# Optimization experiments

Measured on AMD Instinct MI355X. Metric: run time of the kernel, lower is better.

The kernel has to match this reference:

```python
import jax, jax.numpy as jnp
import numpy as np
from jax import lax

H = 2048      # d_inner
N = 8         # half of d_state (conjugate-pair complex modes)
B, L, D_MODEL = 4, 4096, 1024
D_CONV = 4


def setup_inputs() -> dict:
    key = jax.random.key(0)
    ks = jax.random.split(key, 10)
    hidden_states = jax.random.normal(ks[0], (B, L, D_MODEL), dtype=jnp.float32)
    W_in = jax.random.normal(ks[1], (2 * H, D_MODEL), dtype=jnp.float32) / np.sqrt(D_MODEL)
    conv_w = jax.random.normal(ks[2], (H, D_CONV), dtype=jnp.float32) / np.sqrt(D_CONV)
    conv_b = jax.random.normal(ks[3], (H,), dtype=jnp.float32) * 0.1
    # S4D params: dt ~ loguniform(1e-3, 1e-1); A = -0.5 + i*pi*n (legs-ish diag init)
    u = jax.random.uniform(ks[4], (H,), dtype=jnp.float32)
    log_dt = jnp.log(1e-3) + u * (jnp.log(1e-1) - jnp.log(1e-3))
    log_A_real = jnp.log(0.5 * jnp.ones((H, N), dtype=jnp.float32))
    A_imag = jnp.pi * jnp.broadcast_to(jnp.arange(N, dtype=jnp.float32), (H, N)).copy()
    C_re = jax.random.normal(ks[5], (H, N), dtype=jnp.float32)
    C_im = jax.random.normal(ks[6], (H, N), dtype=jnp.float32)
    D = jnp.ones((H,), dtype=jnp.float32)
    W_out = jax.random.normal(ks[7], (D_MODEL, H), dtype=jnp.float32) / np.sqrt(H)
    return dict(hidden_states=hidden_states, W_in=W_in, conv_w=conv_w, conv_b=conv_b,
                log_dt=log_dt, log_A_real=log_A_real, A_imag=A_imag,
                C_re=C_re, C_im=C_im, D=D, W_out=W_out)


def _s4d_kernel(log_dt, log_A_real, A_imag, C_re, C_im, L):
    # S4D (diagonal SSM) convolution kernel, ZOH-style discretization.
    dt = jnp.exp(log_dt)                       # (H,)
    A = -jnp.exp(log_A_real) + 1j * A_imag      # (H,N) complex
    C = C_re + 1j * C_im                        # (H,N)
    dtA = dt[:, None] * A                       # (H,N)
    Ct = C * (jnp.exp(dtA) - 1.0) / A           # (H,N)
    t = jnp.arange(L, dtype=jnp.float32)
    vand = jnp.exp(dtA[:, :, None] * t)         # (H,N,L) Vandermonde
    return 2.0 * jnp.einsum('hn,hnl->hl', Ct, vand).real  # (H,L)


def reference(hidden_states, W_in, conv_w, conv_b, log_dt, log_A_real, A_imag, C_re, C_im, D, W_out):
    B, L, _ = hidden_states.shape
    # in_proj (no bias): (B,L,D) -> (B, 2H, L)
    xz = jnp.einsum('bld,ed->bel', hidden_states, W_in)
    x, z = jnp.split(xz, 2, axis=1)             # each (B,H,L)
    # causal depthwise conv1d + SiLU
    w = conv_w.shape[-1]
    xp = jnp.pad(x, ((0, 0), (0, 0), (w - 1, 0)))
    x = lax.conv_general_dilated(xp, conv_w[:, None, :], (1,), 'VALID',
                                 dimension_numbers=('NCH', 'OIH', 'NCH'),
                                 feature_group_count=x.shape[1])
    x = jax.nn.silu(x + conv_b[None, :, None])
    # S4 FFT long convolution + D skip
    k = _s4d_kernel(log_dt, log_A_real, A_imag, C_re, C_im, L)  # (H,L)
    n = 2 * L
    y = jnp.fft.irfft(jnp.fft.rfft(x, n=n) * jnp.fft.rfft(k, n=n), n=n)[..., :L]
    y = y + x * D[None, :, None]
    # SiLU gate and out_proj
    y = y * jax.nn.silu(z)
    return jnp.einsum('bhl,dh->bld', y, W_out)
```

## Files before the change

### kernel.cpp

```cpp
#include <hip/hip_runtime.h>
#include <hip/hip_bf16.h>
#include <math.h>

#define H_DIM 2048
#define N_ST 8
#define B_SZ 4
#define L_SEQ 4096
#define DMODEL 1024
#define DCONV 4
#define CL 128
#define NC (L_SEQ / CL)

typedef __bf16 bf16x8 __attribute__((ext_vector_type(8)));
typedef __bf16 bf16x4 __attribute__((ext_vector_type(4)));
typedef float f32x4 __attribute__((ext_vector_type(4)));

typedef const unsigned int __attribute__((address_space(1)))* gptr_t;
typedef unsigned int __attribute__((address_space(3)))* lptr_t;

__device__ __forceinline__ void gl_lds16(const __bf16* g, __bf16* l) {
    __builtin_amdgcn_global_load_lds((gptr_t)g, (lptr_t)l, 16, 0, 0);
}

#define WS_XZ     0
#define WS_COEF   16777216
#define WS_STATES 16875520
#define WS_HF     17924096
#define WS_WIF    24215552
#define WS_WOH    30507008
#define WS_WOL    31555584
#define WS_YTL    32604160

__global__ __launch_bounds__(256) void cvt_split4(const float* __restrict__ s,
                                                  __bf16* __restrict__ h,
                                                  __bf16* __restrict__ l, int n4) {
    int i = blockIdx.x * 256 + threadIdx.x;
    if (i >= n4) return;
    float4 v = ((const float4*)s)[i];
    float vv[4] = {v.x, v.y, v.z, v.w};
    bf16x4 hv, lv;
#pragma unroll
    for (int j = 0; j < 4; ++j) {
        __bf16 hb = (__bf16)vv[j];
        hv[j] = hb;
        lv[j] = (__bf16)(vv[j] - (float)hb);
    }
    *(bf16x4*)&h[(size_t)i * 4] = hv;
    *(bf16x4*)&l[(size_t)i * 4] = lv;
}

template <int BSIDE>
__global__ __launch_bounds__(256) void cvt_fuse(const float* __restrict__ s,
                                                __bf16* __restrict__ d, int nOct) {
    int i = blockIdx.x * 256 + threadIdx.x;
    if (i >= nOct) return;
    int row = i >> 7, ko = i & 127;
    const float* p = s + (size_t)row * 1024 + ko * 8;
    float4 v0 = *(const float4*)p;
    float4 v1 = *(const float4*)(p + 4);
    float vv[8] = {v0.x, v0.y, v0.z, v0.w, v1.x, v1.y, v1.z, v1.w};
    bf16x8 hv, lv;
#pragma unroll
    for (int j = 0; j < 8; ++j) {
        __bf16 hb = (__bf16)vv[j];
        hv[j] = hb;
        lv[j] = (__bf16)(vv[j] - (float)hb);
    }
    __bf16* o = d + (size_t)row * 3072 + ko * 24;
    if (BSIDE) {
        *(bf16x8*)(o) = hv; *(bf16x8*)(o + 8) = lv; *(bf16x8*)(o + 16) = hv;
    } else {
        *(bf16x8*)(o) = hv; *(bf16x8*)(o + 8) = hv; *(bf16x8*)(o + 16) = lv;
    }
}

__global__ void coef_kernel(const float* __restrict__ log_dt,
                            const float* __restrict__ log_A_real,
                            const float* __restrict__ A_imag,
                            const float* __restrict__ C_re,
                            const float* __restrict__ C_im,
                            float* __restrict__ coef) {
    int i = blockIdx.x * blockDim.x + threadIdx.x;
    if (i >= H_DIM * N_ST) return;
    int h = i >> 3;
    float dt = expf(log_dt[h]);
    float Ar = -expf(log_A_real[i]);
    float Ai = A_imag[i];
    float er = expf(dt * Ar);
    float ang = dt * Ai;
    float wr = er * cosf(ang);
    float wi = er * sinf(ang);
    float den = Ar * Ar + Ai * Ai;
    float qr = ((wr - 1.f) * Ar + wi * Ai) / den;
    float qi = (wi * Ar - (wr - 1.f) * Ai) / den;
    float Cr = C_re[i], Ci = C_im[i];
    float Ctr = Cr * qr - Ci * qi;
    float Cti = Cr * qi + Ci * qr;
    float eCL = expf((float)CL * dt * Ar);
    float aCL = (float)CL * dt * Ai;
    float pr = eCL * cosf(aCL);
    float pi = eCL * sinf(aCL);
    const int HN = H_DIM * N_ST;
    coef[i]          = wr;
    coef[HN + i]     = wi;
    coef[2 * HN + i] = Ctr;
    coef[3 * HN + i] = Cti;
    coef[4 * HN + i] = pr;
    coef[5 * HN + i] = pi;
}

__global__ __launch_bounds__(512, 2) void gemm_f256p(const __bf16* __restrict__ A,
                                                     const __bf16* __restrict__ B,
                                                     float* __restrict__ C,
                                                     int K, int ldc) {
    __shared__ __bf16 sA[32768], sB[32768];
    const int tid = threadIdx.x;
    const int lane = tid & 63;
    const int wid = tid >> 6;
    const int wrw = wid >> 2, wcw = wid & 3;
    const int bm = blockIdx.y, bn = blockIdx.x;

    f32x4 acc[8][4];
#pragma unroll
    for (int m = 0; m < 8; ++m)
#pragma unroll
        for (int n = 0; n < 4; ++n) acc[m][n] = (f32x4){0.f, 0.f, 0.f, 0.f};

    const int kb = lane >> 4, rr = lane & 15;

    const int f0 = tid, f1 = 512 + tid;
    const int kA0 = f0 >> 8, rA0 = f0 & 255;
    const int kA1 = f1 >> 8, rA1 = f1 & 255;
    const size_t gA0 = (size_t)(bm * 256 + rA0) * K;
    const size_t gA1 = (size_t)(bm * 256 + rA1) * K;
    const size_t gB0 = (size_t)(bn * 256 + rA0) * K;
    const size_t gB1 = (size_t)(bn * 256 + rA1) * K;
    const int dst0 = kA0 * 2048 + rA0 * 8;
    const int dst1 = kA1 * 2048 + rA1 * 8;

    auto stageA = [&](int t, int ks) {
        const int base = (t & 1) * 16384 + ks * 8192;
        const size_t go = (size_t)t * 64 + ks * 32;
        gl_lds16(A + gA0 + go + kA0 * 8, &sA[base + dst0]);
        gl_lds16(A + gA1 + go + kA1 * 8, &sA[base + dst1]);
    };
    auto stageB = [&](int t, int ks) {
        const int base = (t & 1) * 16384 + ks * 8192;
        const size_t go = (size_t)t * 64 + ks * 32;
        gl_lds16(B + gB0 + go + kA0 * 8, &sB[base + dst0]);
        gl_lds16(B + gB1 + go + kA1 * 8, &sB[base + dst1]);
    };

    const int nt = K >> 6;
    stageA(0, 0); stageB(0, 0); stageA(0, 1); stageB(0, 1);
    asm volatile("s_waitcnt vmcnt(0)" ::: "memory");
    __builtin_amdgcn_s_barrier();
    __builtin_amdgcn_sched_barrier(0);

#pragma unroll 1
    for (int t = 0; t < nt; ++t) {
        const int par = (t & 1) * 16384;
        const bool pf = (t + 1 < nt);
        bf16x8 fB[4], fA[4];

        {
            const int bA = par, bB = par;
#pragma unroll
            for (int n = 0; n < 4; ++n)
                fB[n] = *(const bf16x8*)&sB[bB + kb * 2048 + (wcw * 64 + n * 16 + rr) * 8];
#pragma unroll
            for (int m = 0; m < 4; ++m)
                fA[m] = *(const bf16x8*)&sA[bA + kb * 2048 + (wrw * 128 + m * 16 + rr) * 8];
            if (pf) stageA(t + 1, 0);
            __builtin_amdgcn_s_barrier();
            asm volatile("s_waitcnt lgkmcnt(0)" ::: "memory");
            __builtin_amdgcn_sched_barrier(0);
            __builtin_amdgcn_s_setprio(1);
#pragma unroll
            for (int m = 0; m < 4; ++m)
#pragma unroll
                for (int n = 0; n < 4; ++n)
                    acc[m][n] = __builtin_amdgcn_mfma_f32_16x16x32_bf16(fA[m], fB[n], acc[m][n], 0, 0, 0);
            __builtin_amdgcn_s_setprio(0);
            __builtin_amdgcn_s_barrier();
            __builtin_amdgcn_sched_barrier(0);
        }
        {
            const int bA = par;
#pragma unroll
            for (int m = 0; m < 4; ++m)
                fA[m] = *(const bf16x8*)&sA[bA + kb * 2048 + (wrw * 128 + 64 + m * 16 + rr) * 8];
            if (pf) stageB(t + 1, 0);
            __builtin_amdgcn_s_barrier();
            asm volatile("s_waitcnt lgkmcnt(0)" ::: "memory");
            __builtin_amdgcn_sched_barrier(0);
            __builtin_amdgcn_s_setprio(1);
#pragma unroll
            for (int m = 0; m < 4; ++m)
#pragma unroll
                for (int n = 0; n < 4; ++n)
                    acc[4 + m][n] = __builtin_amdgcn_mfma_f32_16x16x32_bf16(fA[m], fB[n], acc[4 + m][n], 0, 0, 0);
            __builtin_amdgcn_s_setprio(0);
            if (pf) asm volatile("s_waitcnt vmcnt(4)" ::: "memory");
            else    asm volatile("s_waitcnt vmcnt(0)" ::: "memory");
            __builtin_amdgcn_s_barrier();
            __builtin_amdgcn_sched_barrier(0);
        }
        {
            const int bA = par + 8192, bB = par + 8192;
#pragma unroll
            for (int n = 0; n < 4; ++n)
                fB[n] = *(const bf16x8*)&sB[bB + kb * 2048 + (wcw * 64 + n * 16 + rr) * 8];
#pragma unroll
            for (int m = 0; m < 4; ++m)
                fA[m] = *(const bf16x8*)&sA[bA + kb * 2048 + (wrw * 128 + m * 16 + rr) * 8];
            if (pf) stageA(t + 1, 1);
            __builtin_amdgcn_s_barrier();
            asm volatile("s_waitcnt lgkmcnt(0)" ::: "memory");
            __builtin_amdgcn_sched_barrier(0);
            __builtin_amdgcn_s_setprio(1);
#pragma unroll
            for (int m = 0; m < 4; ++m)
#pragma unroll
                for (int n = 0; n < 4; ++n)
                    acc[m][n] = __builtin_amdgcn_mfma_f32_16x16x32_bf16(fA[m], fB[n], acc[m][n], 0, 0, 0);
            __builtin_amdgcn_s_setprio(0);
            __builtin_amdgcn_s_barrier();
            __builtin_amdgcn_sched_barrier(0);
        }
        {
            const int bA = par + 8192;
#pragma unroll
            for (int m = 0; m < 4; ++m)
                fA[m] = *(const bf16x8*)&sA[bA + kb * 2048 + (wrw * 128 + 64 + m * 16 + rr) * 8];
            if (pf) stageB(t + 1, 1);
            __builtin_amdgcn_s_barrier();
            asm volatile("s_waitcnt lgkmcnt(0)" ::: "memory");
            __builtin_amdgcn_sched_barrier(0);
            __builtin_amdgcn_s_setprio(1);
#pragma unroll
            for (int m = 0; m < 4; ++m)
#pragma unroll
                for (int n = 0; n < 4; ++n)
                    acc[4 + m][n] = __builtin_amdgcn_mfma_f32_16x16x32_bf16(fA[m], fB[n], acc[4 + m][n], 0, 0, 0);
            __builtin_amdgcn_s_setprio(0);
            if (pf) asm volatile("s_waitcnt vmcnt(4)" ::: "memory");
            else    asm volatile("s_waitcnt vmcnt(0)" ::: "memory");
            __builtin_amdgcn_s_barrier();
            __builtin_amdgcn_sched_barrier(0);
        }
    }

    const int rq = lane >> 4;
#pragma unroll
    for (int m = 0; m < 8; ++m)
#pragma unroll
        for (int n = 0; n < 4; ++n) {
            int col = bn * 256 + wcw * 64 + n * 16 + rr;
            int row0 = bm * 256 + wrw * 128 + m * 16 + rq * 4;
#pragma unroll
            for (int j = 0; j < 4; ++j)
                C[(size_t)(row0 + j) * ldc + col] = acc[m][n][j];
        }
}

__global__ __launch_bounds__(512, 1) void gemm_s128w(const __bf16* __restrict__ Ah,
                                                     const __bf16* __restrict__ Al,
                                                     const __bf16* __restrict__ Bh,
                                                     const __bf16* __restrict__ Bl,
                                                     float* __restrict__ C,
                                                     int K, int ldc) {
    __shared__ __bf16 sAh[2][2][4096], sAl[2][2][4096];
    __shared__ __bf16 sBh[2][2][4096], sBl[2][2][4096];
    const int tid = threadIdx.x;
    const int lane = tid & 63;
    const int wid = tid >> 6;
    const int wrw = wid >> 2;
    const int wcw = wid & 3;
    const int bm = blockIdx.y, bn = blockIdx.x;

    f32x4 acc[4][2];
#pragma unroll
    for (int m = 0; m < 4; ++m)
#pragma unroll
        for (int n = 0; n < 2; ++n) acc[m][n] = (f32x4){0.f, 0.f, 0.f, 0.f};

    const int kb = lane >> 4, rr = lane & 15;

    const int kbs = tid >> 7, rw = tid & 127;
    const size_t gAr = (size_t)(bm * 128 + rw) * K;
    const size_t gBr = (size_t)(bn * 128 + rw) * K;
    const int dd = kbs * 1024 + rw * 8;

    auto stA = [&](int t, int ks) {
        const int par = t & 1;
        const size_t go = (size_t)t * 64 + ks * 32 + kbs * 8;
        gl_lds16(Ah + gAr + go, &sAh[par][ks][dd]);
        gl_lds16(Al + gAr + go, &sAl[par][ks][dd]);
    };
    auto stB = [&](int t, int ks) {
        const int par = t & 1;
        const size_t go = (size_t)t * 64 + ks * 32 + kbs * 8;
        gl_lds16(Bh + gBr + go, &sBh[par][ks][dd]);
        gl_lds16(Bl + gBr + go, &sBl[par][ks][dd]);
    };

    const int nt = K >> 6;
    stA(0, 0); stB(0, 0); stA(0, 1); stB(0, 1);
    asm volatile("s_waitcnt vmcnt(0)" ::: "memory");
    __builtin_amdgcn_s_barrier();
    __builtin_amdgcn_sched_barrier(0);

    bf16x8 fAh[4], fAl[4], fBh[2], fBl[2];

#pragma unroll 1
    for (int t = 0; t < nt; ++t) {
        const int par = t & 1;
        const bool pf = (t + 1 < nt);

        {
#pragma unroll
            for (int n = 0; n < 2; ++n) {
                const int off = kb * 1024 + (wcw * 32 + n * 16 + rr) * 8;
                fBh[n] = *(const bf16x8*)&sBh[par][0][off];
                fBl[n] = *(const bf16x8*)&sBl[par][0][off];
            }
#pragma unroll
            for (int m = 0; m < 4; ++m) {
                const int off = kb * 1024 + (wrw * 64 + m * 16 + rr) * 8;
                fAh[m] = *(const bf16x8*)&sAh[par][0][off];
                fAl[m] = *(const bf16x8*)&sAl[par][0][off];
            }
            if (pf) stA(t + 1, 0);
            __builtin_amdgcn_s_barrier();
            asm volatile("s_waitcnt lgkmcnt(0)" ::: "memory");
            __builtin_amdgcn_sched_barrier(0);
            __builtin_amdgcn_s_setprio(1);
#pragma unroll
            for (int m = 0; m < 2; ++m)
#pragma unroll
                for (int n = 0; n < 2; ++n) {
                    acc[m][n] = __builtin_amdgcn_mfma_f32_16x16x32_bf16(fAh[m], fBh[n], acc[m][n], 0, 0, 0);
                    acc[m][n] = __builtin_amdgcn_mfma_f32_16x16x32_bf16(fAh[m], fBl[n], acc[m][n], 0, 0, 0);
                    acc[m][n] = __builtin_amdgcn_mfma_f32_16x16x32_bf16(fAl[m], fBh[n], acc[m][n], 0, 0, 0);
                }
            __builtin_amdgcn_s_setprio(0);
            __builtin_amdgcn_s_barrier();
            __builtin_amdgcn_sched_barrier(0);
        }
        {
            if (pf) stB(t + 1, 0);
            __builtin_amdgcn_s_barrier();
            __builtin_amdgcn_sched_barrier(0);
            __builtin_amdgcn_s_setprio(1);
#pragma unroll
            for (int m = 2; m < 4; ++m)
#pragma unroll
                for (int n = 0; n < 2; ++n) {
                    acc[m][n] = __builtin_amdgcn_mfma_f32_16x16x32_bf16(fAh[m], fBh[n], acc[m][n], 0, 0, 0);
                    acc[m][n] = __builtin_amdgcn_mfma_f32_16x16x32_bf16(fAh[m], fBl[n], acc[m][n], 0, 0, 0);
                    acc[m][n] = __builtin_amdgcn_mfma_f32_16x16x32_bf16(fAl[m], fBh[n], acc[m][n], 0, 0, 0);
                }
            __builtin_amdgcn_s_setprio(0);
            if (pf) asm volatile("s_waitcnt vmcnt(4)" ::: "memory");
            else    asm volatile("s_waitcnt vmcnt(0)" ::: "memory");
            __builtin_amdgcn_s_barrier();
            __builtin_amdgcn_sched_barrier(0);
        }
        {
#pragma unroll
            for (int n = 0; n < 2; ++n) {
                const int off = kb * 1024 + (wcw * 32 + n * 16 + rr) * 8;
                fBh[n] = *(const bf16x8*)&sBh[par][1][off];
                fBl[n] = *(const bf16x8*)&sBl[par][1][off];
            }
#pragma unroll
            for (int m = 0; m < 4; ++m) {
                const int off = kb * 1024 + (wrw * 64 + m * 16 + rr) * 8;
                fAh[m] = *(const bf16x8*)&sAh[par][1][off];
                fAl[m] = *(const bf16x8*)&sAl[par][1][off];
            }
            if (pf) stA(t + 1, 1);
            __builtin_amdgcn_s_barrier();
            asm volatile("s_waitcnt lgkmcnt(0)" ::: "memory");
            __builtin_amdgcn_sched_barrier(0);
            __builtin_amdgcn_s_setprio(1);
#pragma unroll
            for (int m = 0; m < 2; ++m)
#pragma unroll
                for (int n = 0; n < 2; ++n) {
                    acc[m][n] = __builtin_amdgcn_mfma_f32_16x16x32_bf16(fAh[m], fBh[n], acc[m][n], 0, 0, 0);
                    acc[m][n] = __builtin_amdgcn_mfma_f32_16x16x32_bf16(fAh[m], fBl[n], acc[m][n], 0, 0, 0);
                    acc[m][n] = __builtin_amdgcn_mfma_f32_16x16x32_bf16(fAl[m], fBh[n], acc[m][n], 0, 0, 0);
                }
            __builtin_amdgcn_s_setprio(0);
            __builtin_amdgcn_s_barrier();
            __builtin_amdgcn_sched_barrier(0);
        }
        {
            if (pf) stB(t + 1, 1);
            __builtin_amdgcn_s_barrier();
            __builtin_amdgcn_sched_barrier(0);
            __builtin_amdgcn_s_setprio(1);
#pragma unroll
            for (int m = 2; m < 4; ++m)
#pragma unroll
                for (int n = 0; n < 2; ++n) {
                    acc[m][n] = __builtin_amdgcn_mfma_f32_16x16x32_bf16(fAh[m], fBh[n], acc[m][n], 0, 0, 0);
                    acc[m][n] = __builtin_amdgcn_mfma_f32_16x16x32_bf16(fAh[m], fBl[n], acc[m][n], 0, 0, 0);
                    acc[m][n] = __builtin_amdgcn_mfma_f32_16x16x32_bf16(fAl[m], fBh[n], acc[m][n], 0, 0, 0);
                }
            __builtin_amdgcn_s_setprio(0);
            if (pf) asm volatile("s_waitcnt vmcnt(4)" ::: "memory");
            else    asm volatile("s_waitcnt vmcnt(0)" ::: "memory");
            __builtin_amdgcn_s_barrier();
            __builtin_amdgcn_sched_barrier(0);
        }
    }

    const int rq = lane >> 4;
#pragma unroll
    for (int m = 0; m < 4; ++m)
#pragma unroll
        for (int n = 0; n < 2; ++n) {
            int col = bn * 128 + wcw * 32 + n * 16 + rr;
            int row0 = bm * 128 + wrw * 64 + m * 16 + rq * 4;
#pragma unroll
            for (int j = 0; j < 4; ++j)
                C[(size_t)(row0 + j) * ldc + col] = acc[m][n][j];
        }
}

__global__ __launch_bounds__(256) void scan_phase1(const float* __restrict__ xz,
                                                   const float* __restrict__ coef,
                                                   const float* __restrict__ conv_w,
                                                   const float* __restrict__ conv_b,
                                                   float* __restrict__ states) {
    int t = blockIdx.x * 256 + threadIdx.x;
    int c = t & (NC - 1);
    int h = t >> 5;

    const int HN = H_DIM * N_ST;
    float wr[N_ST], wi[N_ST];
#pragma unroll
    for (int n = 0; n < N_ST; ++n) {
        wr[n] = coef[h * N_ST + n];
        wi[n] = coef[HN + h * N_ST + n];
    }
    float cw0 = conv_w[h * 4 + 0], cw1 = conv_w[h * 4 + 1];
    float cw2 = conv_w[h * 4 + 2], cw3 = conv_w[h * 4 + 3];
    float cb = conv_b[h];

    const float* xrow = xz + (size_t)h * L_SEQ + c * CL;
    float x3 = 0.f, x2 = 0.f, x1 = 0.f;
    if (c > 0) {
        float4 p = *(const float4*)(xrow - 4);
        x3 = p.y; x2 = p.z; x1 = p.w;
    }

    float sr[N_ST], si[N_ST];
#pragma unroll
    for (int n = 0; n < N_ST; ++n) { sr[n] = 0.f; si[n] = 0.f; }

    for (int j = 0; j < CL; j += 4) {
        float4 v = *(const float4*)(xrow + j);
        float xv[4] = {v.x, v.y, v.z, v.w};
#pragma unroll
        for (int k = 0; k < 4; ++k) {
            float u = cw0 * x3 + cw1 * x2 + cw2 * x1 + cw3 * xv[k] + cb;
            float xc = u / (1.f + __expf(-u));
            x3 = x2; x2 = x1; x1 = xv[k];
#pragma unroll
            for (int n = 0; n < N_ST; ++n) {
                float nr = wr[n] * sr[n] - wi[n] * si[n] + xc;
                float ni = wr[n] * si[n] + wi[n] * sr[n];
                sr[n] = nr; si[n] = ni;
            }
        }
    }
    float* st = states + (size_t)t * (N_ST * 2);
#pragma unroll
    for (int n = 0; n < N_ST; ++n) { st[2 * n] = sr[n]; st[2 * n + 1] = si[n]; }
}

__global__ __launch_bounds__(256) void scan_phase2(const float* __restrict__ coef,
                                                   float* __restrict__ states) {
    int h = blockIdx.x * 256 + threadIdx.x;
    if (h >= H_DIM) return;
    const int HN = H_DIM * N_ST;
    float pr[N_ST], pi[N_ST];
#pragma unroll
    for (int n = 0; n < N_ST; ++n) {
        pr[n] = coef[4 * HN + h * N_ST + n];
        pi[n] = coef[5 * HN + h * N_ST + n];
    }
    float sr[N_ST], si[N_ST];
#pragma unroll
    for (int n = 0; n < N_ST; ++n) { sr[n] = 0.f; si[n] = 0.f; }
    float* base = states + (size_t)h * NC * (N_ST * 2);
    for (int c = 0; c < NC; ++c) {
        float* st = base + c * (N_ST * 2);
#pragma unroll
        for (int n = 0; n < N_ST; ++n) {
            float lr = st[2 * n], li = st[2 * n + 1];
            st[2 * n] = sr[n]; st[2 * n + 1] = si[n];
            float nr = pr[n] * sr[n] - pi[n] * si[n] + lr;
            float ni = pr[n] * si[n] + pi[n] * sr[n] + li;
            sr[n] = nr; si[n] = ni;
        }
    }
}

__global__ __launch_bounds__(256) void scan_phase3t(const float* __restrict__ xz,
                                                    const float* __restrict__ coef,
                                                    const float* __restrict__ conv_w,
                                                    const float* __restrict__ conv_b,
                                                    const float* __restrict__ Dvec,
                                                    const float* __restrict__ states,
                                                    __bf16* __restrict__ th,
                                                    __bf16* __restrict__ tl) {
    const int lane = threadIdx.x & 63;
    const int wv = threadIdx.x >> 6;
    const int c = blockIdx.x * 4 + wv;
    const int h = blockIdx.y * 64 + lane;
    const int t = h * NC + c;

    const int HN = H_DIM * N_ST;
    float wr[N_ST], wi[N_ST], Ctr[N_ST], Cti[N_ST];
#pragma unroll
    for (int n = 0; n < N_ST; ++n) {
        wr[n]  = coef[h * N_ST + n];
        wi[n]  = coef[HN + h * N_ST + n];
        Ctr[n] = coef[2 * HN + h * N_ST + n];
        Cti[n] = coef[3 * HN + h * N_ST + n];
    }
    float cw0 = conv_w[h * 4 + 0], cw1 = conv_w[h * 4 + 1];
    float cw2 = conv_w[h * 4 + 2], cw3 = conv_w[h * 4 + 3];
    float cb = conv_b[h];
    float Dh = Dvec[h];

    const float* xrow = xz + (size_t)h * L_SEQ + c * CL;
    const float* zrow = xz + (size_t)(H_DIM + h) * L_SEQ + c * CL;

    float x3 = 0.f, x2 = 0.f, x1 = 0.f;
    if (c > 0) {
        float4 p = *(const float4*)(xrow - 4);
        x3 = p.y; x2 = p.z; x1 = p.w;
    }

    const float* st = states + (size_t)t * (N_ST * 2);
    float sr[N_ST], si[N_ST];
#pragma unroll
    for (int n = 0; n < N_ST; ++n) { sr[n] = st[2 * n]; si[n] = st[2 * n + 1]; }

    __bf16* thp = th + (size_t)(c * CL) * H_DIM + h;
    __bf16* tlp = tl + (size_t)(c * CL) * H_DIM + h;

    for (int j = 0; j < CL; j += 4) {
        float4 v = *(const float4*)(xrow + j);
        float4 zv = *(const float4*)(zrow + j);
        float xv[4] = {v.x, v.y, v.z, v.w};
        float zz[4] = {zv.x, zv.y, zv.z, zv.w};
#pragma unroll
        for (int k = 0; k < 4; ++k) {
            float u = cw0 * x3 + cw1 * x2 + cw2 * x1 + cw3 * xv[k] + cb;
            float xc = u / (1.f + __expf(-u));
            x3 = x2; x2 = x1; x1 = xv[k];
            float accy = 0.f;
#pragma unroll
            for (int n = 0; n < N_ST; ++n) {
                float nr = wr[n] * sr[n] - wi[n] * si[n] + xc;
                float ni = wr[n] * si[n] + wi[n] * sr[n];
                sr[n] = nr; si[n] = ni;
                accy += Ctr[n] * nr - Cti[n] * ni;
            }
            float yv = 2.f * accy + Dh * xc;
            float g = zz[k] / (1.f + __expf(-zz[k]));
            float val = yv * g;
            __bf16 hb = (__bf16)val;
            __bf16 lb = (__bf16)(val - (float)hb);
            thp[(size_t)(j + k) * H_DIM] = hb;
            tlp[(size_t)(j + k) * H_DIM] = lb;
        }
    }
}

extern "C" void kernel_launch(void* const* d_in, const int* in_sizes, int n_in,
                              void* d_out, int out_size, void* d_ws, size_t ws_size,
                              hipStream_t stream) {
    const float* hid        = (const float*)d_in[0];
    const float* W_in       = (const float*)d_in[1];
    const float* conv_w     = (const float*)d_in[2];
    const float* conv_b     = (const float*)d_in[3];
    const float* log_dt     = (const float*)d_in[4];
    const float* log_A_real = (const float*)d_in[5];
    const float* A_imag     = (const float*)d_in[6];
    const float* C_re       = (const float*)d_in[7];
    const float* C_im       = (const float*)d_in[8];
    const float* Dv         = (const float*)d_in[9];
    const float* W_out      = (const float*)d_in[10];
    float* out = (float*)d_out;
    float* ws  = (float*)d_ws;

    float* xz      = ws + WS_XZ;
    float* coef    = ws + WS_COEF;
    float* states  = ws + WS_STATES;
    __bf16* Hf     = (__bf16*)(ws + WS_HF);
    __bf16* WiF    = (__bf16*)(ws + WS_WIF);
    __bf16* Woh    = (__bf16*)(ws + WS_WOH);
    __bf16* Wol    = (__bf16*)(ws + WS_WOL);
    __bf16* yTh    = (__bf16*)(ws + WS_HF);
    __bf16* yTl    = (__bf16*)(ws + WS_YTL);

    coef_kernel<<<(H_DIM * N_ST + 255) / 256, 256, 0, stream>>>(
        log_dt, log_A_real, A_imag, C_re, C_im, coef);

    const int wOct = 2 * H_DIM * DMODEL / 8;
    cvt_fuse<0><<<(wOct + 255) / 256, 256, 0, stream>>>(W_in, WiF, wOct);
    cvt_split4<<<(DMODEL * H_DIM / 4 + 255) / 256, 256, 0, stream>>>(W_out, Woh, Wol, DMODEL * H_DIM / 4);

    const int nscan = H_DIM * NC;
    const int hOct = L_SEQ * DMODEL / 8;
    dim3 gIn(L_SEQ / 256, 2 * H_DIM / 256);
    dim3 gOut(DMODEL / 128, L_SEQ / 128);
    dim3 gP3(NC / 4, H_DIM / 64);

    for (int b = 0; b < B_SZ; ++b) {
        const float* hid_b = hid + (size_t)b * L_SEQ * DMODEL;
        float* out_b = out + (size_t)b * L_SEQ * DMODEL;

        cvt_fuse<1><<<(hOct + 255) / 256, 256, 0, stream>>>(hid_b, Hf, hOct);
        gemm_f256p<<<gIn, 512, 0, stream>>>(WiF, Hf, xz, 3 * DMODEL, L_SEQ);
        scan_phase1<<<nscan / 256, 256, 0, stream>>>(xz, coef, conv_w, conv_b, states);
        scan_phase2<<<(H_DIM + 255) / 256, 256, 0, stream>>>(coef, states);
        scan_phase3t<<<gP3, 256, 0, stream>>>(xz, coef, conv_w, conv_b, Dv, states, yTh, yTl);
        gemm_s128w<<<gOut, 512, 0, stream>>>(yTh, yTl, Woh, Wol, out_b, H_DIM, DMODEL);
    }
}
```

Measured before the change: 1.399 ms.

## Replace 256x256 in_proj GEMM with 128x128 tile, 4-wave kernel

Replaces the 512-thread, 256x256-tile input projection GEMM with a 256-thread, 128x128-tile version that uses a smaller LDS footprint and a 2x2 wave layout. Fragments of A and B are now loaded once per k-substep and reused across two MFMA phases instead of being reloaded. The grid grows fourfold, giving more blocks to fill the CUs. In exchange, each block reuses each loaded tile across fewer outputs, so global/L2 traffic per FLOP goes up.

```diff
diff --git a/kernel.cpp b/kernel.cpp
--- a/kernel.cpp
+++ b/kernel.cpp
@@ -109,75 +109,75 @@
     coef[5 * HN + i] = pi;
 }
 
-__global__ __launch_bounds__(512, 2) void gemm_f256p(const __bf16* __restrict__ A,
-                                                     const __bf16* __restrict__ B,
-                                                     float* __restrict__ C,
-                                                     int K, int ldc) {
-    __shared__ __bf16 sA[32768], sB[32768];
+__global__ __launch_bounds__(256, 2) void gemm_g128(const __bf16* __restrict__ A,
+                                                    const __bf16* __restrict__ B,
+                                                    float* __restrict__ C,
+                                                    int K, int ldc) {
+    __shared__ __bf16 sA[2][2][4096], sB[2][2][4096];
     const int tid = threadIdx.x;
     const int lane = tid & 63;
     const int wid = tid >> 6;
-    const int wrw = wid >> 2, wcw = wid & 3;
+    const int wrw = wid >> 1, wcw = wid & 1;
     const int bm = blockIdx.y, bn = blockIdx.x;
 
-    f32x4 acc[8][4];
-#pragma unroll
-    for (int m = 0; m < 8; ++m)
+    f32x4 acc[4][4];
+#pragma unroll
+    for (int m = 0; m < 4; ++m)
 #pragma unroll
         for (int n = 0; n < 4; ++n) acc[m][n] = (f32x4){0.f, 0.f, 0.f, 0.f};
 
     const int kb = lane >> 4, rr = lane & 15;
 
-    const int f0 = tid, f1 = 512 + tid;
-    const int kA0 = f0 >> 8, rA0 = f0 & 255;
-    const int kA1 = f1 >> 8, rA1 = f1 & 255;
-    const size_t gA0 = (size_t)(bm * 256 + rA0) * K;
-    const size_t gA1 = (size_t)(bm * 256 + rA1) * K;
-    const size_t gB0 = (size_t)(bn * 256 + rA0) * K;
-    const size_t gB1 = (size_t)(bn * 256 + rA1) * K;
-    const int dst0 = kA0 * 2048 + rA0 * 8;
-    const int dst1 = kA1 * 2048 + rA1 * 8;
-
-    auto stageA = [&](int t, int ks) {
-        const int base = (t & 1) * 16384 + ks * 8192;
+    const int o0 = tid, o1 = 256 + tid;
+    const int ko0 = o0 >> 7, rw0 = o0 & 127;
+    const int ko1 = o1 >> 7, rw1 = o1 & 127;
+    const size_t gA0 = (size_t)(bm * 128 + rw0) * K;
+    const size_t gA1 = (size_t)(bm * 128 + rw1) * K;
+    const size_t gB0 = (size_t)(bn * 128 + rw0) * K;
+    const size_t gB1 = (size_t)(bn * 128 + rw1) * K;
+    const int d0 = ko0 * 1024 + rw0 * 8;
+    const int d1 = ko1 * 1024 + rw1 * 8;
+
+    auto stA = [&](int t, int ks) {
+        const int par = t & 1;
         const size_t go = (size_t)t * 64 + ks * 32;
-        gl_lds16(A + gA0 + go + kA0 * 8, &sA[base + dst0]);
-        gl_lds16(A + gA1 + go + kA1 * 8, &sA[base + dst1]);
+        gl_lds16(A + gA0 + go + ko0 * 8, &sA[par][ks][d0]);
+        gl_lds16(A + gA1 + go + ko1 * 8, &sA[par][ks][d1]);
     };
-    auto stageB = [&](int t, int ks) {
-        const int base = (t & 1) * 16384 + ks * 8192;
+    auto stB = [&](int t, int ks) {
+        const int par = t & 1;
         const size_t go = (size_t)t * 64 + ks * 32;
-        gl_lds16(B + gB0 + go + kA0 * 8, &sB[base + dst0]);
-        gl_lds16(B + gB1 + go + kA1 * 8, &sB[base + dst1]);
+        gl_lds16(B + gB0 + go + ko0 * 8, &sB[par][ks][d0]);
+        gl_lds16(B + gB1 + go + ko1 * 8, &sB[par][ks][d1]);
     };
 
     const int nt = K >> 6;
-    stageA(0, 0); stageB(0, 0); stageA(0, 1); stageB(0, 1);
+    stA(0, 0); stB(0, 0); stA(0, 1); stB(0, 1);
     asm volatile("s_waitcnt vmcnt(0)" ::: "memory");
     __builtin_amdgcn_s_barrier();
     __builtin_amdgcn_sched_barrier(0);
 
+    bf16x8 fA[4], fB[4];
+
 #pragma unroll 1
     for (int t = 0; t < nt; ++t) {
-        const int par = (t & 1) * 16384;
+        const int par = t & 1;
         const bool pf = (t + 1 < nt);
-        bf16x8 fB[4], fA[4];
-
-        {
-            const int bA = par, bB = par;
+
+        {
 #pragma unroll
             for (int n = 0; n < 4; ++n)
-                fB[n] = *(const bf16x8*)&sB[bB + kb * 2048 + (wcw * 64 + n * 16 + rr) * 8];
+                fB[n] = *(const bf16x8*)&sB[par][0][kb * 1024 + (wcw * 64 + n * 16 + rr) * 8];
 #pragma unroll
             for (int m = 0; m < 4; ++m)
-                fA[m] = *(const bf16x8*)&sA[bA + kb * 2048 + (wrw * 128 + m * 16 + rr) * 8];
-            if (pf) stageA(t + 1, 0);
+                fA[m] = *(const bf16x8*)&sA[par][0][kb * 1024 + (wrw * 64 + m * 16 + rr) * 8];
+            if (pf) stA(t + 1, 0);
             __builtin_amdgcn_s_barrier();
             asm volatile("s_waitcnt lgkmcnt(0)" ::: "memory");
             __builtin_amdgcn_sched_barrier(0);
             __builtin_amdgcn_s_setprio(1);
 #pragma unroll
-            for (int m = 0; m < 4; ++m)
+            for (int m = 0; m < 2; ++m)
 #pragma unroll
                 for (int n = 0; n < 4; ++n)
                     acc[m][n] = __builtin_amdgcn_mfma_f32_16x16x32_bf16(fA[m], fB[n], acc[m][n], 0, 0, 0);
@@ -186,20 +186,15 @@
             __builtin_amdgcn_sched_barrier(0);
         }
         {
-            const int bA = par;
-#pragma unroll
-            for (int m = 0; m < 4; ++m)
-                fA[m] = *(const bf16x8*)&sA[bA + kb * 2048 + (wrw * 128 + 64 + m * 16 + rr) * 8];
-            if (pf) stageB(t + 1, 0);
-            __builtin_amdgcn_s_barrier();
-            asm volatile("s_waitcnt lgkmcnt(0)" ::: "memory");
-            __builtin_amdgcn_sched_barrier(0);
-            __builtin_amdgcn_s_setprio(1);
-#pragma unroll
-            for (int m = 0; m < 4; ++m)
+            if (pf) stB(t + 1, 0);
+            __builtin_amdgcn_s_barrier();
+            __builtin_amdgcn_sched_barrier(0);
+            __builtin_amdgcn_s_setprio(1);
+#pragma unroll
+            for (int m = 2; m < 4; ++m)
 #pragma unroll
                 for (int n = 0; n < 4; ++n)
-                    acc[4 + m][n] = __builtin_amdgcn_mfma_f32_16x16x32_bf16(fA[m], fB[n], acc[4 + m][n], 0, 0, 0);
+                    acc[m][n] = __builtin_amdgcn_mfma_f32_16x16x32_bf16(fA[m], fB[n], acc[m][n], 0, 0, 0);
             __builtin_amdgcn_s_setprio(0);
             if (pf) asm volatile("s_waitcnt vmcnt(4)" ::: "memory");
             else    asm volatile("s_waitcnt vmcnt(0)" ::: "memory");
@@ -207,20 +202,19 @@
             __builtin_amdgcn_sched_barrier(0);
         }
         {
-            const int bA = par + 8192, bB = par + 8192;
 #pragma unroll
             for (int n = 0; n < 4; ++n)
-                fB[n] = *(const bf16x8*)&sB[bB + kb * 2048 + (wcw * 64 + n * 16 + rr) * 8];
+                fB[n] = *(const bf16x8*)&sB[par][1][kb * 1024 + (wcw * 64 + n * 16 + rr) * 8];
 #pragma unroll
             for (int m = 0; m < 4; ++m)
-                fA[m] = *(const bf16x8*)&sA[bA + kb * 2048 + (wrw * 128 + m * 16 + rr) * 8];
-            if (pf) stageA(t + 1, 1);
+                fA[m] = *(const bf16x8*)&sA[par][1][kb * 1024 + (wrw * 64 + m * 16 + rr) * 8];
+            if (pf) stA(t + 1, 1);
             __builtin_amdgcn_s_barrier();
             asm volatile("s_waitcnt lgkmcnt(0)" ::: "memory");
             __builtin_amdgcn_sched_barrier(0);
             __builtin_amdgcn_s_setprio(1);
 #pragma unroll
-            for (int m = 0; m < 4; ++m)
+            for (int m = 0; m < 2; ++m)
 #pragma unroll
                 for (int n = 0; n < 4; ++n)
                     acc[m][n] = __builtin_amdgcn_mfma_f32_16x16x32_bf16(fA[m], fB[n], acc[m][n], 0, 0, 0);
@@ -229,20 +223,15 @@
             __builtin_amdgcn_sched_barrier(0);
         }
         {
-            const int bA = par + 8192;
-#pragma unroll
-            for (int m = 0; m < 4; ++m)
-                fA[m] = *(const bf16x8*)&sA[bA + kb * 2048 + (wrw * 128 + 64 + m * 16 + rr) * 8];
-            if (pf) stageB(t + 1, 1);
-            __builtin_amdgcn_s_barrier();
-            asm volatile("s_waitcnt lgkmcnt(0)" ::: "memory");
-            __builtin_amdgcn_sched_barrier(0);
-            __builtin_amdgcn_s_setprio(1);
-#pragma unroll
-            for (int m = 0; m < 4; ++m)
+            if (pf) stB(t + 1, 1);
+            __builtin_amdgcn_s_barrier();
+            __builtin_amdgcn_sched_barrier(0);
+            __builtin_amdgcn_s_setprio(1);
+#pragma unroll
+            for (int m = 2; m < 4; ++m)
 #pragma unroll
                 for (int n = 0; n < 4; ++n)
-                    acc[4 + m][n] = __builtin_amdgcn_mfma_f32_16x16x32_bf16(fA[m], fB[n], acc[4 + m][n], 0, 0, 0);
+                    acc[m][n] = __builtin_amdgcn_mfma_f32_16x16x32_bf16(fA[m], fB[n], acc[m][n], 0, 0, 0);
             __builtin_amdgcn_s_setprio(0);
             if (pf) asm volatile("s_waitcnt vmcnt(4)" ::: "memory");
             else    asm volatile("s_waitcnt vmcnt(0)" ::: "memory");
@@ -253,11 +242,11 @@
 
     const int rq = lane >> 4;
 #pragma unroll
-    for (int m = 0; m < 8; ++m)
+    for (int m = 0; m < 4; ++m)
 #pragma unroll
         for (int n = 0; n < 4; ++n) {
-            int col = bn * 256 + wcw * 64 + n * 16 + rr;
-            int row0 = bm * 256 + wrw * 128 + m * 16 + rq * 4;
+            int col = bn * 128 + wcw * 64 + n * 16 + rr;
+            int row0 = bm * 128 + wrw * 64 + m * 16 + rq * 4;
 #pragma unroll
             for (int j = 0; j < 4; ++j)
                 C[(size_t)(row0 + j) * ldc + col] = acc[m][n][j];
@@ -621,7 +610,7 @@
 
     const int nscan = H_DIM * NC;
     const int hOct = L_SEQ * DMODEL / 8;
-    dim3 gIn(L_SEQ / 256, 2 * H_DIM / 256);
+    dim3 gIn(L_SEQ / 128, 2 * H_DIM / 128);
     dim3 gOut(DMODEL / 128, L_SEQ / 128);
     dim3 gP3(NC / 4, H_DIM / 64);
 
@@ -630,7 +619,7 @@
         float* out_b = out + (size_t)b * L_SEQ * DMODEL;
 
         cvt_fuse<1><<<(hOct + 255) / 256, 256, 0, stream>>>(hid_b, Hf, hOct);
-        gemm_f256p<<<gIn, 512, 0, stream>>>(WiF, Hf, xz, 3 * DMODEL, L_SEQ);
+        gemm_g128<<<gIn, 256, 0, stream>>>(WiF, Hf, xz, 3 * DMODEL, L_SEQ);
         scan_phase1<<<nscan / 256, 256, 0, stream>>>(xz, coef, conv_w, conv_b, states);
         scan_phase2<<<(H_DIM + 255) / 256, 256, 0, stream>>>(coef, states);
         scan_phase3t<<<gP3, 256, 0, stream>>>(xz, coef, conv_w, conv_b, Dv, states, yTh, yTl);
```

Measured after the change: 1.687 ms. 1.21x slower.
